# Kernel tuning notes

Measured on AMD Instinct MI355X. Metric: run time of the kernel, lower is better.

The kernel has to match this reference:

```python
import jax, jax.numpy as jnp
import numpy as np

L, E, K = 2, 8, 2  # num_layers, num_experts, top_k
B, S, I, H = 4, 512, 768, 768


def gru_seq(x_seq, h0, Wih, Whh, bih, bhh):
    """PyTorch-semantics GRU over [B,S,H]. Returns (outputs [B,S,H], h_last [B,H])."""
    def step(h, x_t):
        gi = x_t @ Wih.T + bih          # [B,3H]
        gh = h @ Whh.T + bhh            # [B,3H]
        i_r, i_z, i_n = jnp.split(gi, 3, axis=-1)
        h_r, h_z, h_n = jnp.split(gh, 3, axis=-1)
        r = jax.nn.sigmoid(i_r + h_r)
        z = jax.nn.sigmoid(i_z + h_z)
        n = jnp.tanh(i_n + r * h_n)
        h_new = (1.0 - z) * n + z * h
        return h_new, h_new
    h_last, ys = jax.lax.scan(step, h0, jnp.swapaxes(x_seq, 0, 1))  # scan over S
    return jnp.swapaxes(ys, 0, 1), h_last


def setup_inputs() -> dict:
    key = jax.random.key(0)
    ks = jax.random.split(key, 16)
    sc_in = 1.0 / np.sqrt(I)
    sc_h = 1.0 / np.sqrt(H)
    sc_ff = 1.0 / np.sqrt(4 * I)
    return {
        "x": jax.random.normal(ks[0], (B, S, I), jnp.float32),
        "proj_W": jax.random.normal(ks[1], (L, H, I), jnp.float32) * sc_in,
        "proj_b": jnp.zeros((L, H), jnp.float32),
        "gru_Wih": jax.random.normal(ks[2], (3 * H, H), jnp.float32) * sc_h,
        "gru_Whh": jax.random.normal(ks[3], (3 * H, H), jnp.float32) * sc_h,
        "gru_bih": jnp.zeros((3 * H,), jnp.float32),
        "gru_bhh": jnp.zeros((3 * H,), jnp.float32),
        "router_W": jax.random.normal(ks[4], (L, E, H), jnp.float32) * sc_h,
        "router_b": jnp.zeros((L, E), jnp.float32),
        "exp_W1": jax.random.normal(ks[5], (L, E, 4 * I, I), jnp.float32) * sc_in,
        "exp_b1": jnp.zeros((L, E, 4 * I), jnp.float32),
        "exp_W2": jax.random.normal(ks[6], (L, E, I, 4 * I), jnp.float32) * sc_ff,
        "exp_b2": jnp.zeros((L, E, I), jnp.float32),
    }


def reference(x, proj_W, proj_b, gru_Wih, gru_Whh, gru_bih, gru_bhh,
              router_W, router_b, exp_W1, exp_b1, exp_W2, exp_b2):
    h_state = jnp.zeros((B, H), x.dtype)  # GRU state carried across layers
    for l in range(L):
        # layer projection -> recurrent router state
        h_in = x @ proj_W[l].T + proj_b[l]                       # [B,S,H]
        h_seq, h_state = gru_seq(h_in, h_state, gru_Wih, gru_Whh, gru_bih, gru_bhh)
        # top-k routing over experts
        logits = h_seq @ router_W[l].T + router_b[l]             # [B,S,E]
        vals, idx = jax.lax.top_k(logits, K)                     # [B,S,K]
        gates_k = jax.nn.softmax(vals, axis=-1)                  # renormalized over top-k
        gate = jnp.sum(gates_k[..., None] * jax.nn.one_hot(idx, E, dtype=x.dtype), axis=-2)  # [B,S,E]
        # dense-masked expert compute (small fixed E)
        out = jnp.zeros_like(x)
        for e in range(E):
            h1 = jax.nn.relu(x @ exp_W1[l, e].T + exp_b1[l, e])  # [B,S,4I]
            ye = h1 @ exp_W2[l, e].T + exp_b2[l, e]              # [B,S,I]
            out = out + gate[..., e:e + 1] * ye
        x = out
    return x
```

## Files before the change

kernel.cpp:

```cpp
#include <hip/hip_runtime.h>
#include <cmath>

#define AGENT __HIP_MEMORY_SCOPE_AGENT


typedef __attribute__((ext_vector_type(8))) short short8;
typedef __attribute__((ext_vector_type(4))) float f32x4;

__global__ void reset_kernel(int* __restrict__ flags, int* __restrict__ counts,
                             float* __restrict__ hbuf0) {
  int i = blockIdx.x * 256 + threadIdx.x;
  if (i < 6208) flags[i] = 0;
  if (i < 16) counts[i] = 0;
  if (i < 3072) hbuf0[i] = 0.f;
}

__global__ __launch_bounds__(256)
void split_kernel(const float* __restrict__ in, short* __restrict__ hi,
                  short* __restrict__ lo, int n4) {
  int i = blockIdx.x * 256 + threadIdx.x;
  if (i >= n4) return;
  float4 v = ((const float4*)in)[i];
  unsigned ua = __float_as_uint(v.x), ub = __float_as_uint(v.y);
  unsigned uc = __float_as_uint(v.z), ud = __float_as_uint(v.w);
  unsigned ha = ua & 0xFFFF0000u, hb = ub & 0xFFFF0000u;
  unsigned hc = uc & 0xFFFF0000u, hd = ud & 0xFFFF0000u;
  unsigned hp0 = (ua >> 16) | hb;
  unsigned hp1 = (uc >> 16) | hd;
  float la = v.x - __uint_as_float(ha), lb = v.y - __uint_as_float(hb);
  float lc = v.z - __uint_as_float(hc), ld = v.w - __uint_as_float(hd);
  unsigned lp0 = (__float_as_uint(la) >> 16) | (__float_as_uint(lb) & 0xFFFF0000u);
  unsigned lp1 = (__float_as_uint(lc) >> 16) | (__float_as_uint(ld) & 0xFFFF0000u);
  ((uint2*)hi)[i] = make_uint2(hp0, hp1);
  ((uint2*)lo)[i] = make_uint2(lp0, lp1);
}

template<bool GI3>
__global__ __launch_bounds__(256)
void gemm_nt(const float* __restrict__ A, const float* __restrict__ Bw,
             const float* __restrict__ bias, float* __restrict__ C,
             int Kd, int lda, int ldc)
{
  __shared__ float As[16][132];
  __shared__ float Bs[16][132];

  int mbase = blockIdx.y * 128;
  int nbase = blockIdx.x * 128;
  int tid = threadIdx.x;
  int tx = tid & 15, ty = tid >> 4;

  const float* ap[2];
  const float* bp[2];
  int ldst[2];
#pragma unroll
  for (int i = 0; i < 2; ++i) {
    int v = tid + 256 * i;
    int row = v >> 2, kq = v & 3;
    ap[i] = A + (size_t)(mbase + row) * lda + kq * 4;
    bp[i] = Bw + (size_t)(nbase + row) * Kd + kq * 4;
    ldst[i] = kq * 4 * 132 + row;
  }

  float acc[8][8];
#pragma unroll
  for (int i = 0; i < 8; ++i)
#pragma unroll
    for (int j = 0; j < 8; ++j) acc[i][j] = 0.f;

  for (int kb = 0; kb < Kd; kb += 16) {
    float4 av[2], bv[2];
#pragma unroll
    for (int i = 0; i < 2; ++i) {
      av[i] = *(const float4*)(ap[i] + kb);
      bv[i] = *(const float4*)(bp[i] + kb);
    }
    if (kb) __syncthreads();
#pragma unroll
    for (int i = 0; i < 2; ++i) {
      float* ad = &As[0][0] + ldst[i];
      ad[0] = av[i].x; ad[132] = av[i].y; ad[264] = av[i].z; ad[396] = av[i].w;
      float* bd = &Bs[0][0] + ldst[i];
      bd[0] = bv[i].x; bd[132] = bv[i].y; bd[264] = bv[i].z; bd[396] = bv[i].w;
    }
    __syncthreads();
#pragma unroll
    for (int kk = 0; kk < 16; ++kk) {
      float a[8], b[8];
      *(float4*)&a[0] = *(const float4*)&As[kk][ty * 4];
      *(float4*)&a[4] = *(const float4*)&As[kk][ty * 4 + 64];
      *(float4*)&b[0] = *(const float4*)&Bs[kk][tx * 4];
      *(float4*)&b[4] = *(const float4*)&Bs[kk][tx * 4 + 64];
#pragma unroll
      for (int i = 0; i < 8; ++i)
#pragma unroll
        for (int j = 0; j < 8; ++j)
          acc[i][j] = fmaf(a[i], b[j], acc[i][j]);
    }
  }

#pragma unroll
  for (int i = 0; i < 8; ++i) {
    int lrow = ty * 4 + (i & 3) + ((i >> 2) << 6);
    int grow = mbase + lrow;
#pragma unroll
    for (int q = 0; q < 2; ++q) {
      int col = nbase + tx * 4 + (q << 6);
      float4 bb = *(const float4*)&bias[col];
      float4 st = make_float4(acc[i][q * 4 + 0] + bb.x, acc[i][q * 4 + 1] + bb.y,
                              acc[i][q * 4 + 2] + bb.z, acc[i][q * 4 + 3] + bb.w);
      if constexpr (GI3) {
        int t = grow & 511, bb2 = grow >> 9;
        int gate = col / 768, jj = col - gate * 768;
        int wv = jj >> 2;
        float* dst = C + ((((size_t)t * 4 + bb2) * 192 + wv) * 12 + gate * 4);
        *(float4*)dst = st;
      } else {
        *(float4*)&C[(size_t)grow * ldc + col] = st;
      }
    }
  }
}

template<bool SHIFT, bool RELU, bool GATE, bool OUTSPLIT>
__global__ __launch_bounds__(256)
void gemm_mfma(const short* __restrict__ Ah_g, const short* __restrict__ Al_g,
               const float* __restrict__ Bw, const float* __restrict__ bias,
               float* __restrict__ C, short* __restrict__ Ch,
               short* __restrict__ Cl, int Kd, int lda, int ldc,
               const int* __restrict__ list, const int* __restrict__ count,
               const float* __restrict__ gates, long wstride, int bstride)
{
  __shared__ __align__(16) short Ah[128][40];
  __shared__ __align__(16) short Al[128][40];
  __shared__ __align__(16) short Bh[128][40];
  __shared__ __align__(16) short Bl[128][40];
  __shared__ int rowlist[128];

  int e = blockIdx.z;
  int cnt = count[e];
  int mbase = blockIdx.y * 128;
  if (mbase >= cnt) return;
  int nbase = blockIdx.x * 128;
  const float* Bp = Bw + (size_t)e * (size_t)wstride;
  const float* biasp = bias + (size_t)e * (size_t)bstride;

  int tid = threadIdx.x;
  if (tid < 128) {
    int r = mbase + tid;
    rowlist[tid] = list[e * 4096 + (r < cnt ? r : cnt - 1)];
  }
  __syncthreads();

  int arow = tid >> 1, ahalf = tid & 1;
  int aidx0 = rowlist[arow];
  int sr = SHIFT ? (aidx0 >> 1) : aidx0;
  const short* aph = Ah_g + (size_t)sr * lda + ahalf * 16;
  const short* apl = Al_g + (size_t)sr * lda + ahalf * 16;
  const float* bp = Bp + (size_t)(nbase + arow) * Kd + ahalf * 16;

  int wave = tid >> 6, lane = tid & 63;
  int wr = (wave >> 1) * 64, wc = (wave & 1) * 64;
  int fr = lane & 15, fo = (lane >> 4) * 8;

  f32x4 acc[4][4];
#pragma unroll
  for (int i = 0; i < 4; ++i)
#pragma unroll
    for (int j = 0; j < 4; ++j) acc[i][j] = f32x4{0.f, 0.f, 0.f, 0.f};

  for (int kb = 0; kb < Kd; kb += 32) {
    uint4 a_h0 = *(const uint4*)(aph + kb);
    uint4 a_h1 = *(const uint4*)(aph + kb + 8);
    uint4 a_l0 = *(const uint4*)(apl + kb);
    uint4 a_l1 = *(const uint4*)(apl + kb + 8);
    float4 b0 = *(const float4*)(bp + kb);
    float4 b1 = *(const float4*)(bp + kb + 4);
    float4 b2 = *(const float4*)(bp + kb + 8);
    float4 b3 = *(const float4*)(bp + kb + 12);
    if (kb) __syncthreads();
    *(uint4*)&Ah[arow][ahalf * 16] = a_h0;
    *(uint4*)&Ah[arow][ahalf * 16 + 8] = a_h1;
    *(uint4*)&Al[arow][ahalf * 16] = a_l0;
    *(uint4*)&Al[arow][ahalf * 16 + 8] = a_l1;
    unsigned hp[8], lp[8];
    const float4 bbv[4] = {b0, b1, b2, b3};
#pragma unroll
    for (int q = 0; q < 4; ++q) {
      unsigned ua = __float_as_uint(bbv[q].x), ub = __float_as_uint(bbv[q].y);
      unsigned uc = __float_as_uint(bbv[q].z), ud = __float_as_uint(bbv[q].w);
      unsigned ha = ua & 0xFFFF0000u, hb = ub & 0xFFFF0000u;
      unsigned hc = uc & 0xFFFF0000u, hd = ud & 0xFFFF0000u;
      hp[q * 2] = (ua >> 16) | hb;
      hp[q * 2 + 1] = (uc >> 16) | hd;
      float la = bbv[q].x - __uint_as_float(ha);
      float lb = bbv[q].y - __uint_as_float(hb);
      float lc = bbv[q].z - __uint_as_float(hc);
      float ld = bbv[q].w - __uint_as_float(hd);
      lp[q * 2] = (__float_as_uint(la) >> 16) | (__float_as_uint(lb) & 0xFFFF0000u);
      lp[q * 2 + 1] = (__float_as_uint(lc) >> 16) | (__float_as_uint(ld) & 0xFFFF0000u);
    }
    *(uint4*)&Bh[arow][ahalf * 16] = make_uint4(hp[0], hp[1], hp[2], hp[3]);
    *(uint4*)&Bh[arow][ahalf * 16 + 8] = make_uint4(hp[4], hp[5], hp[6], hp[7]);
    *(uint4*)&Bl[arow][ahalf * 16] = make_uint4(lp[0], lp[1], lp[2], lp[3]);
    *(uint4*)&Bl[arow][ahalf * 16 + 8] = make_uint4(lp[4], lp[5], lp[6], lp[7]);
    __syncthreads();

    short8 fah[4], fal[4], fbh[4], fbl[4];
#pragma unroll
    for (int mt = 0; mt < 4; ++mt) {
      fah[mt] = *(const short8*)&Ah[wr + mt * 16 + fr][fo];
      fal[mt] = *(const short8*)&Al[wr + mt * 16 + fr][fo];
    }
#pragma unroll
    for (int nt = 0; nt < 4; ++nt) {
      fbh[nt] = *(const short8*)&Bh[wc + nt * 16 + fr][fo];
      fbl[nt] = *(const short8*)&Bl[wc + nt * 16 + fr][fo];
    }
#pragma unroll
    for (int mt = 0; mt < 4; ++mt)
#pragma unroll
      for (int nt = 0; nt < 4; ++nt) {
        acc[mt][nt] = __builtin_amdgcn_mfma_f32_16x16x32_bf16(fah[mt], fbh[nt], acc[mt][nt], 0, 0, 0);
        acc[mt][nt] = __builtin_amdgcn_mfma_f32_16x16x32_bf16(fah[mt], fbl[nt], acc[mt][nt], 0, 0, 0);
        acc[mt][nt] = __builtin_amdgcn_mfma_f32_16x16x32_bf16(fal[mt], fbh[nt], acc[mt][nt], 0, 0, 0);
      }
  }

  int crow = (lane >> 4) * 4;
#pragma unroll
  for (int mt = 0; mt < 4; ++mt) {
#pragma unroll
    for (int q = 0; q < 4; ++q) {
      int lrow = wr + mt * 16 + crow + q;
      int grow = mbase + lrow;
      if (grow < cnt) {
        int aidx = rowlist[lrow];
#pragma unroll
        for (int nt = 0; nt < 4; ++nt) {
          int col = nbase + wc + nt * 16 + fr;
          float v = acc[mt][nt][q] + biasp[col];
          if (RELU) v = fmaxf(v, 0.f);
          if (GATE) v *= gates[aidx];
          if (OUTSPLIT) {
            unsigned u = __float_as_uint(v);
            unsigned h = u & 0xFFFF0000u;
            Ch[(size_t)aidx * ldc + col] = (short)(u >> 16);
            float l2 = v - __uint_as_float(h);
            Cl[(size_t)aidx * ldc + col] = (short)(__float_as_uint(l2) >> 16);
          } else {
            C[(size_t)aidx * ldc + col] = v;
          }
        }
      }
    }
  }
}

__global__ __launch_bounds__(512, 2)
void gru_kernel(const float* __restrict__ gi3, float* __restrict__ h_seq,
                float* __restrict__ hbuf, const float* __restrict__ Whh,
                const float* __restrict__ bhh,
                int* __restrict__ tags, int stepBase)
{
  const int H = 768, S = 512;
  __shared__ float hs[768];
  int wg = blockIdx.x;
  int b = wg / 24;
  int wgi = wg - b * 24;
  int tid = threadIdx.x;
  int wave = tid >> 6;
  int lane = tid & 63;
  int wv = wgi * 8 + wave;

  float W[4][3][12];
#pragma unroll
  for (int c = 0; c < 4; ++c)
#pragma unroll
    for (int g = 0; g < 3; ++g) {
      const float* wp = Whh + (size_t)(g * H + wv * 4 + c) * H + lane * 4;
      *(float4*)&W[c][g][0] = *(const float4*)(wp);
      *(float4*)&W[c][g][4] = *(const float4*)(wp + 256);
      *(float4*)&W[c][g][8] = *(const float4*)(wp + 512);
    }
  int mycol = wv * 4 + (lane & 3);
  float bh_r = bhh[mycol], bh_z = bhh[H + mycol], bh_n = bhh[2 * H + mycol];

  float h_own = 0.f;
  if (lane < 4)
    h_own = __hip_atomic_load(&hbuf[(stepBase & 1) * 3072 + b * H + mycol],
                              __ATOMIC_RELAXED, AGENT);

  for (int tl = 0; tl < S; ++tl) {
    int g = stepBase + tl;
    const float* hb = hbuf + (g & 1) * 3072 + b * H;
    float* hw = hbuf + ((g + 1) & 1) * 3072 + b * H;

    float gv = 0.f;
    if (lane < 12)
      gv = gi3[((((size_t)tl * 4 + b) * 192 + wv) * 12) + lane];

    if (wave == 0) {
      for (;;) {
        int v1 = (lane < 24)
            ? __hip_atomic_load(&tags[(b * 24 + lane) * 32], __ATOMIC_RELAXED, AGENT)
            : 0x7fffffff;
        if (__all(v1 >= g)) break;
        __builtin_amdgcn_s_sleep(2);
      }
    }
    __syncthreads();

    float4 a = make_float4(0.f, 0.f, 0.f, 0.f);
    if (tid < 192)
      asm volatile("global_load_dwordx4 %0, %1, off sc0 sc1"
                   : "=v"(a) : "v"(hb + tid * 4) : "memory");
    asm volatile("s_waitcnt vmcnt(0)" ::: "memory");
    __builtin_amdgcn_sched_barrier(0);
    if (tid < 192) *(float4*)&hs[tid * 4] = a;
    __syncthreads();

    if (tl >= 1 && tid >= wgi * 8 && tid < wgi * 8 + 8)
      *(float4*)&h_seq[((size_t)b * S + (tl - 1)) * H + tid * 4] = a;

    float hseg[12];
    *(float4*)&hseg[0] = *(const float4*)&hs[lane * 4];
    *(float4*)&hseg[4] = *(const float4*)&hs[256 + lane * 4];
    *(float4*)&hseg[8] = *(const float4*)&hs[512 + lane * 4];

    float acc[4][3];
#pragma unroll
    for (int c = 0; c < 4; ++c)
#pragma unroll
      for (int gg = 0; gg < 3; ++gg) {
        float s = 0.f;
#pragma unroll
        for (int i = 0; i < 12; ++i) s = fmaf(W[c][gg][i], hseg[i], s);
        acc[c][gg] = s;
      }
#pragma unroll
    for (int c = 0; c < 4; ++c)
#pragma unroll
      for (int gg = 0; gg < 3; ++gg) {
        float v = acc[c][gg];
#pragma unroll
        for (int m = 32; m >= 1; m >>= 1) v += __shfl_xor(v, m);
        acc[c][gg] = v;
      }

    float gi_r = __shfl(gv, (lane & 3));
    float gi_z = __shfl(gv, 4 + (lane & 3));
    float gi_n = __shfl(gv, 8 + (lane & 3));

    if (lane < 4) {
      float ar = acc[0][0], az = acc[0][1], an = acc[0][2];
      if (lane == 1) { ar = acc[1][0]; az = acc[1][1]; an = acc[1][2]; }
      if (lane == 2) { ar = acc[2][0]; az = acc[2][1]; an = acc[2][2]; }
      if (lane == 3) { ar = acc[3][0]; az = acc[3][1]; an = acc[3][2]; }
      float r = 1.f / (1.f + expf(-(gi_r + ar + bh_r)));
      float z = 1.f / (1.f + expf(-(gi_z + az + bh_z)));
      float n = tanhf(gi_n + r * (an + bh_n));
      float hn = (1.f - z) * n + z * h_own;
      h_own = hn;
      __hip_atomic_store(&hw[mycol], hn, __ATOMIC_RELAXED, AGENT);
    }

    asm volatile("s_waitcnt vmcnt(0)" ::: "memory");
    __syncthreads();
    if (tid == 0)
      __hip_atomic_store(&tags[(b * 24 + wgi) * 32], g + 1, __ATOMIC_RELAXED, AGENT);
  }

  if (lane < 4)
    h_seq[((size_t)b * S + (S - 1)) * H + mycol] = h_own;
}

__global__ __launch_bounds__(64)
void router_kernel(const float* __restrict__ h_seq, const float* __restrict__ rW,
                   const float* __restrict__ rb, int* __restrict__ counts,
                   int* __restrict__ lists, float* __restrict__ gates)
{
  int t = blockIdx.x;
  int lane = threadIdx.x;
  const float* hp = h_seq + (size_t)t * 768 + lane * 12;
  float h[12];
  *(float4*)&h[0] = *(const float4*)(hp);
  *(float4*)&h[4] = *(const float4*)(hp + 4);
  *(float4*)&h[8] = *(const float4*)(hp + 8);

  float lg[8];
#pragma unroll
  for (int e = 0; e < 8; ++e) {
    const float* wp = rW + e * 768 + lane * 12;
    float s = 0.f;
#pragma unroll
    for (int i = 0; i < 12; ++i) s = fmaf(h[i], wp[i], s);
#pragma unroll
    for (int m = 32; m >= 1; m >>= 1) s += __shfl_xor(s, m);
    lg[e] = s + rb[e];
  }
  if (lane == 0) {
    float v1 = lg[0]; int e1 = 0;
#pragma unroll
    for (int e = 1; e < 8; ++e) {
      if (lg[e] > v1) { v1 = lg[e]; e1 = e; }
    }
    float v2 = -INFINITY; int es = 0;
#pragma unroll
    for (int e = 0; e < 8; ++e) {
      if (e != e1 && lg[e] > v2) { v2 = lg[e]; es = e; }
    }
    float ed = expf(v2 - v1);
    float g1 = 1.f / (1.f + ed);
    float g2 = ed / (1.f + ed);
    int a0 = t * 2, a1 = t * 2 + 1;
    gates[a0] = g1;
    gates[a1] = g2;
    int p = atomicAdd(&counts[e1], 1);
    lists[e1 * 4096 + p] = a0;
    p = atomicAdd(&counts[es], 1);
    lists[es * 4096 + p] = a1;
  }
}

__global__ __launch_bounds__(256)
void combine_kernel(const float* __restrict__ ybuf, float* __restrict__ out)
{
  int i = blockIdx.x * 256 + threadIdx.x;
  int fi = i * 4;
  int t = fi / 768;
  int d = fi % 768;
  float4 y0 = *(const float4*)&ybuf[(size_t)(2 * t) * 768 + d];
  float4 y1 = *(const float4*)&ybuf[(size_t)(2 * t + 1) * 768 + d];
  float4 r = make_float4(y0.x + y1.x, y0.y + y1.y, y0.z + y1.z, y0.w + y1.w);
  *(float4*)&out[fi] = r;
}

extern "C" void kernel_launch(void* const* d_in, const int* in_sizes, int n_in,
                              void* d_out, int out_size, void* d_ws, size_t ws_size,
                              hipStream_t stream) {
  (void)in_sizes; (void)n_in; (void)out_size; (void)ws_size;
  const float* x      = (const float*)d_in[0];
  const float* proj_W = (const float*)d_in[1];
  const float* proj_b = (const float*)d_in[2];
  const float* Wih    = (const float*)d_in[3];
  const float* Whh    = (const float*)d_in[4];
  const float* bih    = (const float*)d_in[5];
  const float* bhh    = (const float*)d_in[6];
  const float* rW     = (const float*)d_in[7];
  const float* rb     = (const float*)d_in[8];
  const float* eW1    = (const float*)d_in[9];
  const float* eb1    = (const float*)d_in[10];
  const float* eW2    = (const float*)d_in[11];
  const float* eb2    = (const float*)d_in[12];
  float* out = (float*)d_out;

  float* f = (float*)d_ws;
  float* h_in  = f;
  float* gi3   = h_in + 1572864;
  float* h_seq = gi3 + 4718592;
  float* x_buf = h_seq + 1572864;
  float* ybuf  = x_buf + 1572864;
  float* hbuf  = ybuf + 3145728;
  float* gates = hbuf + 6144;
  short* xh    = (short*)(gates + 4096);
  short* xl    = xh + 1572864;
  short* H1h   = xl + 1572864;
  short* H1l   = H1h + 12582912;
  int* ints    = (int*)(H1l + 12582912);
  int* counts  = ints;
  int* lists   = ints + 16;
  int* tags    = ints + 16 + 32768;

  reset_kernel<<<25, 256, 0, stream>>>(tags, counts, hbuf);

  for (int l = 0; l < 2; ++l) {
    const float* xin = l ? x_buf : x;

    dim3 g1(6, 16);
    gemm_nt<false><<<g1, 256, 0, stream>>>(
        xin, proj_W + (size_t)l * 768 * 768, proj_b + l * 768, h_in,
        768, 768, 768);

    dim3 g2(18, 16);
    gemm_nt<true><<<g2, 256, 0, stream>>>(
        h_in, Wih, bih, gi3, 768, 768, 0);

    gru_kernel<<<96, 512, 0, stream>>>(gi3, h_seq, hbuf, Whh, bhh,
                                       tags, l * 512);

    router_kernel<<<2048, 64, 0, stream>>>(h_seq, rW + (size_t)l * 8 * 768,
                                           rb + l * 8, counts + l * 8, lists, gates);

    split_kernel<<<1536, 256, 0, stream>>>(xin, xh, xl, 393216);

    dim3 ga(24, 32, 8);
    gemm_mfma<true, true, false, true><<<ga, 256, 0, stream>>>(
        xh, xl, eW1 + (size_t)l * 8 * 3072 * 768, eb1 + (size_t)l * 8 * 3072,
        nullptr, H1h, H1l, 768, 768, 3072,
        lists, counts + l * 8, nullptr, (long)3072 * 768, 3072);

    dim3 gb(6, 32, 8);
    gemm_mfma<false, false, true, false><<<gb, 256, 0, stream>>>(
        H1h, H1l, eW2 + (size_t)l * 8 * 768 * 3072, eb2 + (size_t)l * 8 * 768,
        ybuf, nullptr, nullptr, 3072, 3072, 768,
        lists, counts + l * 8, gates, (long)768 * 3072, 768);

    combine_kernel<<<1536, 256, 0, stream>>>(ybuf, l ? out : x_buf);
  }
}
```

Measured before the change: 5.449 ms.

## Replace GRU flag barrier with NaN-sentinel per-step hidden state buffers

```diff
diff --git a/kernel.cpp b/kernel.cpp
--- a/kernel.cpp
+++ b/kernel.cpp
@@ -7,12 +7,26 @@
 typedef __attribute__((ext_vector_type(8))) short short8;
 typedef __attribute__((ext_vector_type(4))) float f32x4;
 
-__global__ void reset_kernel(int* __restrict__ flags, int* __restrict__ counts,
-                             float* __restrict__ hbuf0) {
+__global__ __launch_bounds__(256)
+void reset_kernel(float* __restrict__ hstep, float* __restrict__ zbuf,
+                  int* __restrict__ counts) {
   int i = blockIdx.x * 256 + threadIdx.x;
-  if (i < 6208) flags[i] = 0;
+  if (i < 786432) {
+    float qn = __uint_as_float(0x7FC00000u);
+    float* p = hstep + (size_t)i * 4;
+    __hip_atomic_store(p + 0, qn, __ATOMIC_RELAXED, AGENT);
+    __hip_atomic_store(p + 1, qn, __ATOMIC_RELAXED, AGENT);
+    __hip_atomic_store(p + 2, qn, __ATOMIC_RELAXED, AGENT);
+    __hip_atomic_store(p + 3, qn, __ATOMIC_RELAXED, AGENT);
+  }
+  if (i < 768) {
+    float* p = zbuf + (size_t)i * 4;
+    __hip_atomic_store(p + 0, 0.f, __ATOMIC_RELAXED, AGENT);
+    __hip_atomic_store(p + 1, 0.f, __ATOMIC_RELAXED, AGENT);
+    __hip_atomic_store(p + 2, 0.f, __ATOMIC_RELAXED, AGENT);
+    __hip_atomic_store(p + 3, 0.f, __ATOMIC_RELAXED, AGENT);
+  }
   if (i < 16) counts[i] = 0;
-  if (i < 3072) hbuf0[i] = 0.f;
 }
 
 __global__ __launch_bounds__(256)
@@ -258,9 +272,8 @@
 
 __global__ __launch_bounds__(512, 2)
 void gru_kernel(const float* __restrict__ gi3, float* __restrict__ h_seq,
-                float* __restrict__ hbuf, const float* __restrict__ Whh,
-                const float* __restrict__ bhh,
-                int* __restrict__ tags, int stepBase)
+                float* __restrict__ hstep, const float* __restrict__ hprev,
+                const float* __restrict__ Whh, const float* __restrict__ bhh)
 {
   const int H = 768, S = 512;
   __shared__ float hs[768];
@@ -287,34 +300,31 @@
 
   float h_own = 0.f;
   if (lane < 4)
-    h_own = __hip_atomic_load(&hbuf[(stepBase & 1) * 3072 + b * H + mycol],
-                              __ATOMIC_RELAXED, AGENT);
+    h_own = __hip_atomic_load(&hprev[b * H + mycol], __ATOMIC_RELAXED, AGENT);
 
   for (int tl = 0; tl < S; ++tl) {
-    int g = stepBase + tl;
-    const float* hb = hbuf + (g & 1) * 3072 + b * H;
-    float* hw = hbuf + ((g + 1) & 1) * 3072 + b * H;
-
     float gv = 0.f;
     if (lane < 12)
       gv = gi3[((((size_t)tl * 4 + b) * 192 + wv) * 12) + lane];
 
-    if (wave == 0) {
-      for (;;) {
-        int v1 = (lane < 24)
-            ? __hip_atomic_load(&tags[(b * 24 + lane) * 32], __ATOMIC_RELAXED, AGENT)
-            : 0x7fffffff;
-        if (__all(v1 >= g)) break;
-        __builtin_amdgcn_s_sleep(2);
+    float4 a = make_float4(0.f, 0.f, 0.f, 0.f);
+    if (tid < 192) {
+      if (tl == 0) {
+        asm volatile("global_load_dwordx4 %0, %1, off sc0 sc1"
+                     : "=v"(a) : "v"(hprev + b * 768 + tid * 4) : "memory");
+        asm volatile("s_waitcnt vmcnt(0)" ::: "memory");
+      } else {
+        const float* src = hstep + ((size_t)(tl - 1) * 4 + b) * 768 + tid * 4;
+        for (;;) {
+          asm volatile("global_load_dwordx4 %0, %1, off sc0 sc1"
+                       : "=v"(a) : "v"(src) : "memory");
+          asm volatile("s_waitcnt vmcnt(0)" ::: "memory");
+          if (!((a.x != a.x) | (a.y != a.y) | (a.z != a.z) | (a.w != a.w)))
+            break;
+          __builtin_amdgcn_s_sleep(1);
+        }
       }
     }
-    __syncthreads();
-
-    float4 a = make_float4(0.f, 0.f, 0.f, 0.f);
-    if (tid < 192)
-      asm volatile("global_load_dwordx4 %0, %1, off sc0 sc1"
-                   : "=v"(a) : "v"(hb + tid * 4) : "memory");
-    asm volatile("s_waitcnt vmcnt(0)" ::: "memory");
     __builtin_amdgcn_sched_barrier(0);
     if (tid < 192) *(float4*)&hs[tid * 4] = a;
     __syncthreads();
@@ -326,6 +336,7 @@
     *(float4*)&hseg[0] = *(const float4*)&hs[lane * 4];
     *(float4*)&hseg[4] = *(const float4*)&hs[256 + lane * 4];
     *(float4*)&hseg[8] = *(const float4*)&hs[512 + lane * 4];
+    __syncthreads();
 
     float acc[4][3];
 #pragma unroll
@@ -361,13 +372,9 @@
       float n = tanhf(gi_n + r * (an + bh_n));
       float hn = (1.f - z) * n + z * h_own;
       h_own = hn;
-      __hip_atomic_store(&hw[mycol], hn, __ATOMIC_RELAXED, AGENT);
-    }
-
-    asm volatile("s_waitcnt vmcnt(0)" ::: "memory");
-    __syncthreads();
-    if (tid == 0)
-      __hip_atomic_store(&tags[(b * 24 + wgi) * 32], g + 1, __ATOMIC_RELAXED, AGENT);
+      __hip_atomic_store(&hstep[((size_t)tl * 4 + b) * 768 + mycol], hn,
+                         __ATOMIC_RELAXED, AGENT);
+    }
   }
 
   if (lane < 4)
@@ -460,8 +467,9 @@
   float* h_seq = gi3 + 4718592;
   float* x_buf = h_seq + 1572864;
   float* ybuf  = x_buf + 1572864;
-  float* hbuf  = ybuf + 3145728;
-  float* gates = hbuf + 6144;
+  float* hstep = ybuf + 3145728;
+  float* zbuf  = hstep + 3145728;
+  float* gates = zbuf + 3072;
   short* xh    = (short*)(gates + 4096);
   short* xl    = xh + 1572864;
   short* H1h   = xl + 1572864;
@@ -469,12 +477,13 @@
   int* ints    = (int*)(H1l + 12582912);
   int* counts  = ints;
   int* lists   = ints + 16;
-  int* tags    = ints + 16 + 32768;
-
-  reset_kernel<<<25, 256, 0, stream>>>(tags, counts, hbuf);
+
+  reset_kernel<<<3072, 256, 0, stream>>>(hstep, zbuf, counts);
 
   for (int l = 0; l < 2; ++l) {
     const float* xin = l ? x_buf : x;
+    float* hstepL = hstep + (size_t)l * 1572864;
+    const float* hprevL = l ? (hstep + (size_t)511 * 3072) : zbuf;
 
     dim3 g1(6, 16);
     gemm_nt<false><<<g1, 256, 0, stream>>>(
@@ -485,8 +494,7 @@
     gemm_nt<true><<<g2, 256, 0, stream>>>(
         h_in, Wih, bih, gi3, 768, 768, 0);
 
-    gru_kernel<<<96, 512, 0, stream>>>(gi3, h_seq, hbuf, Whh, bhh,
-                                       tags, l * 512);
+    gru_kernel<<<96, 512, 0, stream>>>(gi3, h_seq, hstepL, hprevL, Whh, bhh);
 
     router_kernel<<<2048, 64, 0, stream>>>(h_seq, rW + (size_t)l * 8 * 768,
                                            rb + l * 8, counts + l * 8, lists, gates);
```

Result: faster. 4.926 ms (-9.6%).
